# Kernel tuning notes

Hardware: AMD Instinct MI355X
Metric: run time of the kernel (lower is better)

Reference implementation:

```python
import jax, jax.numpy as jnp
import numpy as np

N_NODES = 100000
N_EDGES = 1600000
FEAT, HID, OUT = 256, 128, 64
N_BATCH = 10000
EPS = 1e-5


def gcn_conv(x, src, dst, W, b, n):
    # PyG GCNConv: linear -> add self loops -> sym-normalized scatter-add -> bias
    h = x @ W  # [N, C]
    loop = jnp.arange(n, dtype=src.dtype)
    s = jnp.concatenate([src, loop])
    d = jnp.concatenate([dst, loop])
    deg = jax.ops.segment_sum(jnp.ones_like(d, dtype=h.dtype), d, num_segments=n)
    dinv = jnp.where(deg > 0, jax.lax.rsqrt(deg), 0.0)
    norm = dinv[s] * dinv[d]                    # [E+N]
    msg = h[s] * norm[:, None]                  # gather + scale
    out = jax.ops.segment_sum(msg, d, num_segments=n)  # scatter-add
    return out + b


def batch_norm(x, gamma, beta):
    # training-mode BatchNorm1d: batch statistics, biased variance
    mu = jnp.mean(x, axis=0)
    var = jnp.var(x, axis=0)
    return (x - mu) * jax.lax.rsqrt(var + EPS) * gamma + beta


def setup_inputs() -> dict:
    key = jax.random.key(0)
    ks = jax.random.split(key, 8)
    features = jax.random.normal(ks[0], (N_NODES, FEAT), dtype=jnp.float32)
    edge_index = jax.random.randint(ks[1], (2, N_EDGES), 0, N_NODES, dtype=jnp.int64 if jax.config.jax_enable_x64 else jnp.int32)
    batch_nodes = jax.random.randint(ks[2], (N_BATCH,), 0, N_NODES, dtype=jnp.int32)
    W1 = jax.random.normal(ks[3], (FEAT, HID), dtype=jnp.float32) * (1.0 / np.sqrt(FEAT))
    b1 = jnp.zeros((HID,), jnp.float32)
    gamma1 = jnp.ones((HID,), jnp.float32)
    beta1 = jnp.zeros((HID,), jnp.float32)
    W2 = jax.random.normal(ks[4], (HID, OUT), dtype=jnp.float32) * (1.0 / np.sqrt(HID))
    b2 = jnp.zeros((OUT,), jnp.float32)
    gamma2 = jnp.ones((OUT,), jnp.float32)
    beta2 = jnp.zeros((OUT,), jnp.float32)
    return {"features": features, "edge_index": edge_index, "batch_nodes": batch_nodes,
            "W1": W1, "b1": b1, "gamma1": gamma1, "beta1": beta1,
            "W2": W2, "b2": b2, "gamma2": gamma2, "beta2": beta2}


def reference(features, edge_index, batch_nodes, W1, b1, gamma1, beta1, W2, b2, gamma2, beta2):
    src, dst = edge_index[0], edge_index[1]
    n = features.shape[0]
    x = gcn_conv(features, src, dst, W1, b1, n)
    x = jax.nn.relu(batch_norm(x, gamma1, beta1))
    # dropout treated as identity (deterministic reference)
    x = gcn_conv(x, src, dst, W2, b2, n)
    x = jax.nn.relu(batch_norm(x, gamma2, beta2))
    return jax.nn.log_softmax(x[batch_nodes], axis=1)
```

## Files before the change

### kernel.cpp

```cpp
#include <hip/hip_runtime.h>
#include <stdint.h>

typedef unsigned short bf16_t;

constexpr int kNN   = 100000;
constexpr int kNE   = 1600000;
constexpr int kFEAT = 256;
constexpr int kHID  = 128;
constexpr int kOUT  = 64;
constexpr int kNB   = 10000;
constexpr float kEPS = 1e-5f;

constexpr int kEPB  = 4096;
constexpr int kNBLK = (kNE + kEPB - 1) / kEPB;
constexpr int kNBUK = (kNN + 511) / 512;

typedef __attribute__((ext_vector_type(8))) short short8v;
typedef __attribute__((ext_vector_type(4))) float f32x4;

__device__ __forceinline__ float bf2f(bf16_t u) {
    union { uint32_t i; float f; } v; v.i = ((uint32_t)u) << 16; return v.f;
}
__device__ __forceinline__ bf16_t f2bf(float f) {
    uint32_t u = __float_as_uint(f);
    uint32_t r = (u + 0x7FFFu + ((u >> 16) & 1u)) >> 16;
    return (bf16_t)r;
}
__device__ __forceinline__ float lo16(uint32_t u) {
    union { uint32_t i; float f; } v; v.i = u << 16; return v.f;
}
__device__ __forceinline__ float hi16(uint32_t u) {
    union { uint32_t i; float f; } v; v.i = u & 0xFFFF0000u; return v.f;
}

__global__ void k_probe(const uint32_t* __restrict__ feat, const uint32_t* __restrict__ ei,
                        int* __restrict__ flags) {
    if (blockIdx.x == 0 && threadIdx.x == 0) {
        int good = 0;
        for (int j = 0; j < 256; j++) {
            uint32_t u = feat[j];
            uint32_t e = (u >> 7) & 0xFFu;
            if (e >= 100u && e <= 132u) good++;
        }
        flags[0] = (good > 128) ? 1 : 0;
        int zeros = 0;
        for (int j = 0; j < 128; j++) {
            if (ei[2 * j + 1] == 0u) zeros++;
        }
        flags[1] = (zeros > 64) ? 1 : 0;
    }
}


__global__ void k_hist1(const int* __restrict__ ei, const int* __restrict__ flags,
                        unsigned int* __restrict__ counts) {
    __shared__ unsigned int lh[kNBUK];
    int t = threadIdx.x;
    for (int i = t; i < kNBUK; i += 256) lh[i] = 0u;
    __syncthreads();
    int i64 = flags[1];
    int base = blockIdx.x * kEPB;
    for (int k = 0; k < 16; k++) {
        int e = base + k * 256 + t;
        if (e < kNE) {
            int d = i64 ? ei[2 * (kNE + e)] : ei[kNE + e];
            atomicAdd(&lh[d >> 9], 1u);
        }
    }
    __syncthreads();
    for (int i = t; i < kNBUK; i += 256) counts[(size_t)i * kNBLK + blockIdx.x] = lh[i];
}

__global__ void k_scanA(const unsigned int* __restrict__ counts, unsigned int* __restrict__ base,
                        float* __restrict__ stats) {
    __shared__ unsigned int ss[256];
    int t = threadIdx.x;
    for (int i = t; i < 384; i += 256) stats[i] = 0.f;
    unsigned int tot = 0u;
    if (t < kNBUK) {
        const unsigned int* row = counts + (size_t)t * kNBLK;
        for (int j = 0; j < kNBLK; j++) tot += row[j];
    }
    ss[t] = tot;
    __syncthreads();
    for (int o = 1; o < 256; o <<= 1) {
        unsigned int x = (t >= o) ? ss[t - o] : 0u;
        __syncthreads();
        ss[t] += x;
        __syncthreads();
    }
    if (t < kNBUK) base[t] = ss[t] - tot;
    if (t == 0) base[kNBUK] = ss[255];
}

__global__ void k_scanB(const unsigned int* __restrict__ counts, const unsigned int* __restrict__ base,
                        unsigned int* __restrict__ off) {
    __shared__ unsigned int ss[64];
    int b = blockIdx.x, t = threadIdx.x;
    unsigned int run = base[b];
    for (int c0 = 0; c0 < kNBLK; c0 += 64) {
        int idx = c0 + t;
        unsigned int v = (idx < kNBLK) ? counts[(size_t)b * kNBLK + idx] : 0u;
        ss[t] = v;
        __syncthreads();
        for (int o = 1; o < 64; o <<= 1) {
            unsigned int x = (t >= o) ? ss[t - o] : 0u;
            __syncthreads();
            ss[t] += x;
            __syncthreads();
        }
        if (idx < kNBLK) off[(size_t)b * kNBLK + idx] = run + ss[t] - v;
        unsigned int ctot = ss[63];
        __syncthreads();
        run += ctot;
    }
}

__global__ void k_scatter1(const int* __restrict__ ei, const int* __restrict__ flags,
                           const unsigned int* __restrict__ off, unsigned int* __restrict__ pairs) {
    __shared__ unsigned int lcur[kNBUK];
    int t = threadIdx.x;
    for (int i = t; i < kNBUK; i += 256) lcur[i] = off[(size_t)i * kNBLK + blockIdx.x];
    __syncthreads();
    int i64 = flags[1];
    int base = blockIdx.x * kEPB;
    for (int k = 0; k < 16; k++) {
        int e = base + k * 256 + t;
        if (e < kNE) {
            int s, d;
            if (i64) { s = ei[2 * e]; d = ei[2 * (kNE + e)]; }
            else     { s = ei[e];     d = ei[kNE + e]; }
            unsigned int p = atomicAdd(&lcur[d >> 9], 1u);
            pairs[p] = (unsigned int)s | ((unsigned int)(d & 511) << 17);
        }
    }
}

__global__ void __launch_bounds__(1024) k_scatter2(const unsigned int* __restrict__ pairs,
                        const unsigned int* __restrict__ base, unsigned int* __restrict__ deg,
                        float* __restrict__ dinv, unsigned int* __restrict__ cursor,
                        int* __restrict__ sorted) {
    __shared__ unsigned int hist[512], sc[512], lcur[512];
    int b = blockIdx.x, t = threadIdx.x;
    unsigned int gb = base[b];
    int cnt = (int)(base[b + 1] - gb);
    if (t < 512) hist[t] = 0u;
    __syncthreads();
    for (int i = t; i < cnt; i += 1024) atomicAdd(&hist[pairs[gb + i] >> 17], 1u);
    __syncthreads();
    if (t < 512) sc[t] = hist[t];
    __syncthreads();
    for (int o = 1; o < 512; o <<= 1) {
        unsigned int x = 0u;
        if (t < 512 && t >= o) x = sc[t - o];
        __syncthreads();
        if (t < 512) sc[t] += x;
        __syncthreads();
    }
    if (t < 512) {
        lcur[t] = gb + sc[t] - hist[t];
        int node = b * 512 + t;
        if (node < kNN) {
            unsigned int dg = hist[t] + 1u;
            deg[node] = dg;
            dinv[node] = rsqrtf((float)dg);
            cursor[node] = gb + sc[t];
        }
    }
    __syncthreads();
    for (int i = t; i < cnt; i += 1024) {
        unsigned int pk = pairs[gb + i];
        unsigned int slot = atomicAdd(&lcur[pk >> 17], 1u);
        sorted[slot] = (int)(pk & 0x1FFFFu);
    }
}


__global__ void k_prepw1(const void* __restrict__ W, const int* __restrict__ flags,
                         bf16_t* __restrict__ Wz) {
    int idx = blockIdx.x * 256 + threadIdx.x;
    if (idx >= 8 * 8 * 64) return;
    int l = idx & 63;
    int j = (idx >> 6) & 7;
    int t = idx >> 9;
    int col = j * 16 + (l & 15);
    int kb = t * 32 + (l >> 4) * 8;
    bf16_t o[8];
    if (flags[0]) {
        const bf16_t* Wb = (const bf16_t*)W;
        #pragma unroll
        for (int i = 0; i < 8; i++) o[i] = Wb[(size_t)(kb + i) * kHID + col];
    } else {
        const float* Wf = (const float*)W;
        #pragma unroll
        for (int i = 0; i < 8; i++) o[i] = f2bf(Wf[(size_t)(kb + i) * kHID + col]);
    }
    uint4 w;
    w.x = (uint32_t)o[0] | ((uint32_t)o[1] << 16);
    w.y = (uint32_t)o[2] | ((uint32_t)o[3] << 16);
    w.z = (uint32_t)o[4] | ((uint32_t)o[5] << 16);
    w.w = (uint32_t)o[6] | ((uint32_t)o[7] << 16);
    *(uint4*)(Wz + (size_t)idx * 8) = w;
}

__global__ void k_prepw2(const void* __restrict__ W, const int* __restrict__ flags,
                         bf16_t* __restrict__ Wz) {
    int idx = blockIdx.x * 256 + threadIdx.x;
    if (idx >= 4 * 4 * 64) return;
    int l = idx & 63;
    int j = (idx >> 6) & 3;
    int t = idx >> 8;
    int col = j * 16 + (l & 15);
    int kb = t * 32 + (l >> 4) * 8;
    bf16_t o[8];
    if (flags[0]) {
        const bf16_t* Wb = (const bf16_t*)W;
        #pragma unroll
        for (int i = 0; i < 8; i++) o[i] = Wb[(size_t)(kb + i) * kOUT + col];
    } else {
        const float* Wf = (const float*)W;
        #pragma unroll
        for (int i = 0; i < 8; i++) o[i] = f2bf(Wf[(size_t)(kb + i) * kOUT + col]);
    }
    uint4 w;
    w.x = (uint32_t)o[0] | ((uint32_t)o[1] << 16);
    w.y = (uint32_t)o[2] | ((uint32_t)o[3] << 16);
    w.z = (uint32_t)o[4] | ((uint32_t)o[5] << 16);
    w.w = (uint32_t)o[6] | ((uint32_t)o[7] << 16);
    *(uint4*)(Wz + (size_t)idx * 8) = w;
}

__global__ void k_gemm1(const void* __restrict__ A, const bf16_t* __restrict__ Wz,
                        const float* __restrict__ dinv, bf16_t* __restrict__ H,
                        const int* __restrict__ flags) {
    int isbf = flags[0];
    int wv = threadIdx.x >> 6;
    int l  = threadIdx.x & 63;
    int kgrp = l >> 4;
    int rbase = blockIdx.x * 128 + wv * 32;
    int arow0 = rbase + (l & 15);
    int arow1 = arow0 + 16;
    const bf16_t* Ab = (const bf16_t*)A;
    const float*  Af = (const float*)A;
    const short8v* Wv = (const short8v*)Wz;

    f32x4 acc[2][8];
    #pragma unroll
    for (int m = 0; m < 2; m++)
        #pragma unroll
        for (int j = 0; j < 8; j++)
            acc[m][j] = (f32x4){0.f, 0.f, 0.f, 0.f};

    #pragma unroll
    for (int t = 0; t < 8; t++) {
        int kbase = t * 32 + kgrp * 8;
        short8v a0, a1;
        #pragma unroll
        for (int i = 0; i < 8; i++) { a0[i] = 0; a1[i] = 0; }
        if (arow0 < kNN) {
            if (isbf) {
                a0 = *(const short8v*)(Ab + (size_t)arow0 * kFEAT + kbase);
            } else {
                const float* p = Af + (size_t)arow0 * kFEAT + kbase;
                #pragma unroll
                for (int i = 0; i < 8; i++) a0[i] = (short)f2bf(p[i]);
            }
        }
        if (arow1 < kNN) {
            if (isbf) {
                a1 = *(const short8v*)(Ab + (size_t)arow1 * kFEAT + kbase);
            } else {
                const float* p = Af + (size_t)arow1 * kFEAT + kbase;
                #pragma unroll
                for (int i = 0; i < 8; i++) a1[i] = (short)f2bf(p[i]);
            }
        }
        #pragma unroll
        for (int j = 0; j < 8; j++) {
            short8v b = Wv[(t * 8 + j) * 64 + l];
            acc[0][j] = __builtin_amdgcn_mfma_f32_16x16x32_bf16(a0, b, acc[0][j], 0, 0, 0);
            acc[1][j] = __builtin_amdgcn_mfma_f32_16x16x32_bf16(a1, b, acc[1][j], 0, 0, 0);
        }
    }

    #pragma unroll
    for (int m = 0; m < 2; m++) {
        #pragma unroll
        for (int r = 0; r < 4; r++) {
            int orow = rbase + m * 16 + kgrp * 4 + r;
            if (orow < kNN) {
                float dn = dinv[orow];
                bf16_t* hp = H + (size_t)orow * kHID + (l & 15);
                #pragma unroll
                for (int j = 0; j < 8; j++) hp[j * 16] = f2bf(acc[m][j][r] * dn);
            }
        }
    }
}

__global__ void k_agg1(const bf16_t* __restrict__ H, const int* __restrict__ sorted,
                       const unsigned int* __restrict__ cursor, const unsigned int* __restrict__ deg,
                       const float* __restrict__ dinv, const void* __restrict__ bias,
                       const int* __restrict__ flags, float* __restrict__ Out) {
    int t = threadIdx.x;
    int local = t >> 6;
    int lane = t & 63;
    int c0 = lane * 2;
    int n = blockIdx.x * 4 + local;
    if (n >= kNN) return;
    const uint32_t* Hrow = (const uint32_t*)H;
    float dn = dinv[n];
    uint32_t hu = Hrow[(size_t)n * 64 + lane];
    float acc0 = lo16(hu), acc1 = hi16(hu);
    unsigned int e1 = cursor[n];
    unsigned int e = e1 - (deg[n] - 1u);
    int cnt = (int)(e1 - e);
    for (; cnt >= 4; cnt -= 4, e += 4) {
        int s0 = sorted[e], s1 = sorted[e + 1], s2 = sorted[e + 2], s3 = sorted[e + 3];
        uint32_t u0 = Hrow[(size_t)s0 * 64 + lane];
        uint32_t u1 = Hrow[(size_t)s1 * 64 + lane];
        uint32_t u2 = Hrow[(size_t)s2 * 64 + lane];
        uint32_t u3 = Hrow[(size_t)s3 * 64 + lane];
        acc0 += lo16(u0) + lo16(u1) + lo16(u2) + lo16(u3);
        acc1 += hi16(u0) + hi16(u1) + hi16(u2) + hi16(u3);
    }
    for (; cnt > 0; cnt--, e++) {
        uint32_t u = Hrow[(size_t)sorted[e] * 64 + lane];
        acc0 += lo16(u);
        acc1 += hi16(u);
    }
    float b0, b1v;
    if (flags[0]) { b0 = bf2f(((const bf16_t*)bias)[c0]); b1v = bf2f(((const bf16_t*)bias)[c0 + 1]); }
    else          { b0 = ((const float*)bias)[c0];        b1v = ((const float*)bias)[c0 + 1]; }
    float2 o; o.x = acc0 * dn + b0; o.y = acc1 * dn + b1v;
    *(float2*)(Out + (size_t)n * kHID + c0) = o;
}

__global__ void k_stat1(const float* __restrict__ A1, float* __restrict__ stats) {
    int c = threadIdx.x & 127;
    int r0 = threadIdx.x >> 7;
    int chunk = (kNN + gridDim.x - 1) / gridDim.x;
    int nbeg = blockIdx.x * chunk;
    int nend = nbeg + chunk; if (nend > kNN) nend = kNN;
    float s0 = 0.f, s1 = 0.f;
    for (int n = nbeg + r0; n < nend; n += 2) {
        float v = A1[(size_t)n * kHID + c];
        s0 += v; s1 += v * v;
    }
    atomicAdd(&stats[c], s0);
    atomicAdd(&stats[kHID + c], s1);
}

__global__ void k_bnrelu1(const float* __restrict__ A1, const float* __restrict__ stats,
                          const void* __restrict__ gamma, const void* __restrict__ beta,
                          const int* __restrict__ flags, bf16_t* __restrict__ X1) {
    size_t i = (size_t)blockIdx.x * 256 + threadIdx.x;
    if (i >= (size_t)kNN * kHID) return;
    int c = (int)(i & 127);
    float mu = stats[c] * (1.f / kNN);
    float var = stats[kHID + c] * (1.f / kNN) - mu * mu;
    float g, b;
    if (flags[0]) { g = bf2f(((const bf16_t*)gamma)[c]); b = bf2f(((const bf16_t*)beta)[c]); }
    else          { g = ((const float*)gamma)[c];        b = ((const float*)beta)[c]; }
    float v = (A1[i] - mu) * rsqrtf(var + kEPS) * g + b;
    X1[i] = f2bf(v > 0.f ? v : 0.f);
}

__global__ void k_gemm2(const bf16_t* __restrict__ A, const bf16_t* __restrict__ Wz,
                        const float* __restrict__ dinv, bf16_t* __restrict__ H) {
    int wv = threadIdx.x >> 6;
    int l  = threadIdx.x & 63;
    int kgrp = l >> 4;
    int rbase = blockIdx.x * 128 + wv * 32;
    int arow0 = rbase + (l & 15);
    int arow1 = arow0 + 16;
    const short8v* Wv = (const short8v*)Wz;

    f32x4 acc[2][4];
    #pragma unroll
    for (int m = 0; m < 2; m++)
        #pragma unroll
        for (int j = 0; j < 4; j++)
            acc[m][j] = (f32x4){0.f, 0.f, 0.f, 0.f};

    #pragma unroll
    for (int t = 0; t < 4; t++) {
        int kbase = t * 32 + kgrp * 8;
        short8v a0, a1;
        #pragma unroll
        for (int i = 0; i < 8; i++) { a0[i] = 0; a1[i] = 0; }
        if (arow0 < kNN) a0 = *(const short8v*)(A + (size_t)arow0 * kHID + kbase);
        if (arow1 < kNN) a1 = *(const short8v*)(A + (size_t)arow1 * kHID + kbase);
        #pragma unroll
        for (int j = 0; j < 4; j++) {
            short8v b = Wv[(t * 4 + j) * 64 + l];
            acc[0][j] = __builtin_amdgcn_mfma_f32_16x16x32_bf16(a0, b, acc[0][j], 0, 0, 0);
            acc[1][j] = __builtin_amdgcn_mfma_f32_16x16x32_bf16(a1, b, acc[1][j], 0, 0, 0);
        }
    }

    #pragma unroll
    for (int m = 0; m < 2; m++) {
        #pragma unroll
        for (int r = 0; r < 4; r++) {
            int orow = rbase + m * 16 + kgrp * 4 + r;
            if (orow < kNN) {
                float dn = dinv[orow];
                bf16_t* hp = H + (size_t)orow * kOUT + (l & 15);
                #pragma unroll
                for (int j = 0; j < 4; j++) hp[j * 16] = f2bf(acc[m][j][r] * dn);
            }
        }
    }
}

__global__ void k_agg2(const bf16_t* __restrict__ H, const int* __restrict__ sorted,
                       const unsigned int* __restrict__ cursor, const unsigned int* __restrict__ deg,
                       const float* __restrict__ dinv, const void* __restrict__ bias,
                       const int* __restrict__ flags, float* __restrict__ Out) {
    int t = threadIdx.x;
    int local = t >> 5;
    int lane = t & 31;
    int c0 = lane * 2;
    int n = blockIdx.x * 8 + local;
    if (n >= kNN) return;
    const uint32_t* Hrow = (const uint32_t*)H;
    float dn = dinv[n];
    uint32_t hu = Hrow[(size_t)n * 32 + lane];
    float acc0 = lo16(hu), acc1 = hi16(hu);
    unsigned int e1 = cursor[n];
    unsigned int e = e1 - (deg[n] - 1u);
    int cnt = (int)(e1 - e);
    for (; cnt >= 4; cnt -= 4, e += 4) {
        int s0 = sorted[e], s1 = sorted[e + 1], s2 = sorted[e + 2], s3 = sorted[e + 3];
        uint32_t u0 = Hrow[(size_t)s0 * 32 + lane];
        uint32_t u1 = Hrow[(size_t)s1 * 32 + lane];
        uint32_t u2 = Hrow[(size_t)s2 * 32 + lane];
        uint32_t u3 = Hrow[(size_t)s3 * 32 + lane];
        acc0 += lo16(u0) + lo16(u1) + lo16(u2) + lo16(u3);
        acc1 += hi16(u0) + hi16(u1) + hi16(u2) + hi16(u3);
    }
    for (; cnt > 0; cnt--, e++) {
        uint32_t u = Hrow[(size_t)sorted[e] * 32 + lane];
        acc0 += lo16(u);
        acc1 += hi16(u);
    }
    float b0, b1v;
    if (flags[0]) { b0 = bf2f(((const bf16_t*)bias)[c0]); b1v = bf2f(((const bf16_t*)bias)[c0 + 1]); }
    else          { b0 = ((const float*)bias)[c0];        b1v = ((const float*)bias)[c0 + 1]; }
    float2 o; o.x = acc0 * dn + b0; o.y = acc1 * dn + b1v;
    *(float2*)(Out + (size_t)n * kOUT + c0) = o;
}

__global__ void k_stat2(const float* __restrict__ A2, float* __restrict__ stats) {
    int c = threadIdx.x & 63;
    int r0 = threadIdx.x >> 6;
    int chunk = (kNN + gridDim.x - 1) / gridDim.x;
    int nbeg = blockIdx.x * chunk;
    int nend = nbeg + chunk; if (nend > kNN) nend = kNN;
    float s0 = 0.f, s1 = 0.f;
    for (int n = nbeg + r0; n < nend; n += 4) {
        float v = A2[(size_t)n * kOUT + c];
        s0 += v; s1 += v * v;
    }
    atomicAdd(&stats[256 + c], s0);
    atomicAdd(&stats[320 + c], s1);
}

__global__ void k_out(const float* __restrict__ A2, const float* __restrict__ stats,
                      const int* __restrict__ batch, const void* __restrict__ gamma,
                      const void* __restrict__ beta, const int* __restrict__ flags,
                      bf16_t* __restrict__ out) {
    int wid = threadIdx.x >> 6;
    int lane = threadIdx.x & 63;
    int i = blockIdx.x * 4 + wid;
    if (i >= kNB) return;
    int n = batch[i];
    int c = lane;
    float mu = stats[256 + c] * (1.f / kNN);
    float var = stats[320 + c] * (1.f / kNN) - mu * mu;
    float g, b;
    if (flags[0]) { g = bf2f(((const bf16_t*)gamma)[c]); b = bf2f(((const bf16_t*)beta)[c]); }
    else          { g = ((const float*)gamma)[c];        b = ((const float*)beta)[c]; }
    float v = (A2[(size_t)n * kOUT + c] - mu) * rsqrtf(var + kEPS) * g + b;
    v = v > 0.f ? v : 0.f;
    float m = v;
    for (int o = 32; o; o >>= 1) m = fmaxf(m, __shfl_xor(m, o));
    float ex = expf(v - m);
    float s = ex;
    for (int o = 32; o; o >>= 1) s += __shfl_xor(s, o);
    float r = v - m - logf(s);
    if (flags[0]) out[(size_t)i * kOUT + c] = f2bf(r);
    else ((float*)out)[(size_t)i * kOUT + c] = r;
}

static inline size_t align_up(size_t x, size_t a) { return (x + a - 1) & ~(a - 1); }

extern "C" void kernel_launch(void* const* d_in, const int* in_sizes, int n_in,
                              void* d_out, int out_size, void* d_ws, size_t ws_size,
                              hipStream_t stream) {
    (void)in_sizes; (void)n_in; (void)out_size; (void)ws_size;
    const void* feat = d_in[0];
    const int* ei    = (const int*)d_in[1];
    const int* batch = (const int*)d_in[2];
    const void* W1   = d_in[3];
    const void* b1   = d_in[4];
    const void* g1   = d_in[5];
    const void* be1  = d_in[6];
    const void* W2   = d_in[7];
    const void* b2   = d_in[8];
    const void* g2   = d_in[9];
    const void* be2  = d_in[10];

    char* ws = (char*)d_ws;
    size_t o = 0;
    int*          flags  = (int*)(ws + o);          o = align_up(o + 32, 256);
    unsigned int* deg    = (unsigned int*)(ws + o); o = align_up(o + (size_t)kNN * 4, 256);
    float*        dinv   = (float*)(ws + o);        o = align_up(o + (size_t)kNN * 4, 256);
    unsigned int* cursor = (unsigned int*)(ws + o); o = align_up(o + (size_t)kNN * 4, 256);
    float*        stats  = (float*)(ws + o);        o = align_up(o + 384 * 4, 256);
    int*          sorted = (int*)(ws + o);          o = align_up(o + (size_t)kNE * 4, 256);
    bf16_t*       h1     = (bf16_t*)(ws + o);       o = align_up(o + (size_t)kNN * kHID * 2, 256);
    float*        a1     = (float*)(ws + o);        o = align_up(o + (size_t)kNN * kHID * 4, 256);
    bf16_t*       wz1    = (bf16_t*)(ws + o);       o = align_up(o + (size_t)8 * 8 * 64 * 8 * 2, 256);
    bf16_t*       wz2    = (bf16_t*)(ws + o);       o = align_up(o + (size_t)4 * 4 * 64 * 8 * 2, 256);

    unsigned int* pairs  = (unsigned int*)h1;
    unsigned int* counts = (unsigned int*)a1;
    unsigned int* offm   = (unsigned int*)((char*)a1 + 512 * 1024);
    unsigned int* gbase  = (unsigned int*)((char*)a1 + 1024 * 1024);

    bf16_t*       x1 = h1;
    bf16_t*       h2 = (bf16_t*)a1;
    float*        a2 = (float*)((char*)a1 + 16u * 1024u * 1024u);

    bf16_t* outp = (bf16_t*)d_out;

    k_probe   <<<1, 64, 0, stream>>>((const uint32_t*)feat, (const uint32_t*)ei, flags);
    k_prepw1  <<<16, 256, 0, stream>>>(W1, flags, wz1);
    k_prepw2  <<<4, 256, 0, stream>>>(W2, flags, wz2);
    k_hist1   <<<kNBLK, 256, 0, stream>>>(ei, flags, counts);
    k_scanA   <<<1, 256, 0, stream>>>(counts, gbase, stats);
    k_scanB   <<<kNBUK, 64, 0, stream>>>(counts, gbase, offm);
    k_scatter1<<<kNBLK, 256, 0, stream>>>(ei, flags, offm, pairs);
    k_scatter2<<<kNBUK, 1024, 0, stream>>>(pairs, gbase, deg, dinv, cursor, sorted);

    k_gemm1  <<<(kNN + 127) / 128, 256, 0, stream>>>(feat, wz1, dinv, h1, flags);
    k_agg1   <<<(kNN + 3) / 4, 256, 0, stream>>>(h1, sorted, cursor, deg, dinv, b1, flags, a1);
    k_stat1  <<<256, 256, 0, stream>>>(a1, stats);
    k_bnrelu1<<<(kNN * kHID + 255) / 256, 256, 0, stream>>>(a1, stats, g1, be1, flags, x1);

    k_gemm2<<<(kNN + 127) / 128, 256, 0, stream>>>(x1, wz2, dinv, h2);
    k_agg2 <<<(kNN + 7) / 8, 256, 0, stream>>>(h2, sorted, cursor, deg, dinv, b2, flags, a2);
    k_stat2<<<256, 256, 0, stream>>>(a2, stats);

    k_out<<<(kNB + 3) / 4, 256, 0, stream>>>(a2, stats, batch, g2, be2, flags, outp);
}
```

Baseline: 533.6 us.

## Fuse BN stats into aggregation and BN+ReLU into second GEMM load

The aggregation kernels now accumulate per-channel sum and sum-of-squares in shared memory and flush them with atomics, which removes the separate stat passes. BatchNorm+ReLU for layer 1 is folded into the second GEMM's A-operand load through a precomputed scale/shift vector, which drops the bnrelu kernel and the bf16 intermediate. The gathers move to 16-byte loads per lane, with indices shared by shuffles within a 16- or 8-lane group, and the grid becomes grid-stride. The weight-prep kernels are merged and the probe is parallelised. The trade-offs are that the GEMM2 A read is now fp32 (twice the bytes), h2 uses a padded 256-element stride, and every node issues many shared-memory atomics.

```diff
diff --git a/kernel.cpp b/kernel.cpp
--- a/kernel.cpp
+++ b/kernel.cpp
@@ -33,20 +33,26 @@
     union { uint32_t i; float f; } v; v.i = u & 0xFFFF0000u; return v.f;
 }
 
+#define ACC8(u) do { \
+    acc[0] += lo16((u).x); acc[1] += hi16((u).x); \
+    acc[2] += lo16((u).y); acc[3] += hi16((u).y); \
+    acc[4] += lo16((u).z); acc[5] += hi16((u).z); \
+    acc[6] += lo16((u).w); acc[7] += hi16((u).w); } while (0)
+
 __global__ void k_probe(const uint32_t* __restrict__ feat, const uint32_t* __restrict__ ei,
                         int* __restrict__ flags) {
-    if (blockIdx.x == 0 && threadIdx.x == 0) {
-        int good = 0;
-        for (int j = 0; j < 256; j++) {
-            uint32_t u = feat[j];
-            uint32_t e = (u >> 7) & 0xFFu;
-            if (e >= 100u && e <= 132u) good++;
-        }
+    int l = threadIdx.x;
+    int good = 0;
+    for (int j = l; j < 256; j += 64) {
+        uint32_t e = (feat[j] >> 7) & 0xFFu;
+        if (e >= 100u && e <= 132u) good++;
+    }
+    for (int o = 32; o; o >>= 1) good += __shfl_xor(good, o);
+    int zeros = 0;
+    for (int j = l; j < 128; j += 64) zeros += (ei[2 * j + 1] == 0u) ? 1 : 0;
+    for (int o = 32; o; o >>= 1) zeros += __shfl_xor(zeros, o);
+    if (l == 0) {
         flags[0] = (good > 128) ? 1 : 0;
-        int zeros = 0;
-        for (int j = 0; j < 128; j++) {
-            if (ei[2 * j + 1] == 0u) zeros++;
-        }
         flags[1] = (zeros > 64) ? 1 : 0;
     }
 }
@@ -175,59 +181,54 @@
     }
 }
 
-
-__global__ void k_prepw1(const void* __restrict__ W, const int* __restrict__ flags,
-                         bf16_t* __restrict__ Wz) {
-    int idx = blockIdx.x * 256 + threadIdx.x;
-    if (idx >= 8 * 8 * 64) return;
-    int l = idx & 63;
-    int j = (idx >> 6) & 7;
-    int t = idx >> 9;
-    int col = j * 16 + (l & 15);
-    int kb = t * 32 + (l >> 4) * 8;
-    bf16_t o[8];
-    if (flags[0]) {
-        const bf16_t* Wb = (const bf16_t*)W;
-        #pragma unroll
-        for (int i = 0; i < 8; i++) o[i] = Wb[(size_t)(kb + i) * kHID + col];
-    } else {
-        const float* Wf = (const float*)W;
-        #pragma unroll
-        for (int i = 0; i < 8; i++) o[i] = f2bf(Wf[(size_t)(kb + i) * kHID + col]);
-    }
-    uint4 w;
-    w.x = (uint32_t)o[0] | ((uint32_t)o[1] << 16);
-    w.y = (uint32_t)o[2] | ((uint32_t)o[3] << 16);
-    w.z = (uint32_t)o[4] | ((uint32_t)o[5] << 16);
-    w.w = (uint32_t)o[6] | ((uint32_t)o[7] << 16);
-    *(uint4*)(Wz + (size_t)idx * 8) = w;
-}
-
-__global__ void k_prepw2(const void* __restrict__ W, const int* __restrict__ flags,
-                         bf16_t* __restrict__ Wz) {
-    int idx = blockIdx.x * 256 + threadIdx.x;
-    if (idx >= 4 * 4 * 64) return;
-    int l = idx & 63;
-    int j = (idx >> 6) & 3;
-    int t = idx >> 8;
-    int col = j * 16 + (l & 15);
-    int kb = t * 32 + (l >> 4) * 8;
-    bf16_t o[8];
-    if (flags[0]) {
-        const bf16_t* Wb = (const bf16_t*)W;
-        #pragma unroll
-        for (int i = 0; i < 8; i++) o[i] = Wb[(size_t)(kb + i) * kOUT + col];
-    } else {
-        const float* Wf = (const float*)W;
-        #pragma unroll
-        for (int i = 0; i < 8; i++) o[i] = f2bf(Wf[(size_t)(kb + i) * kOUT + col]);
-    }
-    uint4 w;
-    w.x = (uint32_t)o[0] | ((uint32_t)o[1] << 16);
-    w.y = (uint32_t)o[2] | ((uint32_t)o[3] << 16);
-    w.z = (uint32_t)o[4] | ((uint32_t)o[5] << 16);
-    w.w = (uint32_t)o[6] | ((uint32_t)o[7] << 16);
-    *(uint4*)(Wz + (size_t)idx * 8) = w;
+__global__ void k_prepw(const void* __restrict__ W1, const void* __restrict__ W2,
+                        const int* __restrict__ flags, bf16_t* __restrict__ Wz1,
+                        bf16_t* __restrict__ Wz2) {
+    int gid = blockIdx.x * 256 + threadIdx.x;
+    int isbf = flags[0];
+    if (gid < 4096) {
+        int idx = gid;
+        int l = idx & 63, j = (idx >> 6) & 7, t = idx >> 9;
+        int col = j * 16 + (l & 15);
+        int kb = t * 32 + (l >> 4) * 8;
+        bf16_t o[8];
+        if (isbf) {
+            const bf16_t* Wb = (const bf16_t*)W1;
+            #pragma unroll
+            for (int i = 0; i < 8; i++) o[i] = Wb[(size_t)(kb + i) * kHID + col];
+        } else {
+            const float* Wf = (const float*)W1;
+            #pragma unroll
+            for (int i = 0; i < 8; i++) o[i] = f2bf(Wf[(size_t)(kb + i) * kHID + col]);
+        }
+        uint4 w;
+        w.x = (uint32_t)o[0] | ((uint32_t)o[1] << 16);
+        w.y = (uint32_t)o[2] | ((uint32_t)o[3] << 16);
+        w.z = (uint32_t)o[4] | ((uint32_t)o[5] << 16);
+        w.w = (uint32_t)o[6] | ((uint32_t)o[7] << 16);
+        *(uint4*)(Wz1 + (size_t)idx * 8) = w;
+    } else if (gid < 4096 + 1024) {
+        int idx = gid - 4096;
+        int l = idx & 63, j = (idx >> 6) & 3, t = idx >> 8;
+        int col = j * 16 + (l & 15);
+        int kb = t * 32 + (l >> 4) * 8;
+        bf16_t o[8];
+        if (isbf) {
+            const bf16_t* Wb = (const bf16_t*)W2;
+            #pragma unroll
+            for (int i = 0; i < 8; i++) o[i] = Wb[(size_t)(kb + i) * kOUT + col];
+        } else {
+            const float* Wf = (const float*)W2;
+            #pragma unroll
+            for (int i = 0; i < 8; i++) o[i] = f2bf(Wf[(size_t)(kb + i) * kOUT + col]);
+        }
+        uint4 w;
+        w.x = (uint32_t)o[0] | ((uint32_t)o[1] << 16);
+        w.y = (uint32_t)o[2] | ((uint32_t)o[3] << 16);
+        w.z = (uint32_t)o[4] | ((uint32_t)o[5] << 16);
+        w.w = (uint32_t)o[6] | ((uint32_t)o[7] << 16);
+        *(uint4*)(Wz2 + (size_t)idx * 8) = w;
+    }
 }
 
 __global__ void k_gemm1(const void* __restrict__ A, const bf16_t* __restrict__ Wz,
@@ -301,73 +302,94 @@
 __global__ void k_agg1(const bf16_t* __restrict__ H, const int* __restrict__ sorted,
                        const unsigned int* __restrict__ cursor, const unsigned int* __restrict__ deg,
                        const float* __restrict__ dinv, const void* __restrict__ bias,
-                       const int* __restrict__ flags, float* __restrict__ Out) {
+                       const int* __restrict__ flags, float* __restrict__ Out,
+                       float* __restrict__ stats) {
+    __shared__ float ss[256];
     int t = threadIdx.x;
-    int local = t >> 6;
-    int lane = t & 63;
-    int c0 = lane * 2;
-    int n = blockIdx.x * 4 + local;
-    if (n >= kNN) return;
-    const uint32_t* Hrow = (const uint32_t*)H;
-    float dn = dinv[n];
-    uint32_t hu = Hrow[(size_t)n * 64 + lane];
-    float acc0 = lo16(hu), acc1 = hi16(hu);
-    unsigned int e1 = cursor[n];
-    unsigned int e = e1 - (deg[n] - 1u);
-    int cnt = (int)(e1 - e);
-    for (; cnt >= 4; cnt -= 4, e += 4) {
-        int s0 = sorted[e], s1 = sorted[e + 1], s2 = sorted[e + 2], s3 = sorted[e + 3];
-        uint32_t u0 = Hrow[(size_t)s0 * 64 + lane];
-        uint32_t u1 = Hrow[(size_t)s1 * 64 + lane];
-        uint32_t u2 = Hrow[(size_t)s2 * 64 + lane];
-        uint32_t u3 = Hrow[(size_t)s3 * 64 + lane];
-        acc0 += lo16(u0) + lo16(u1) + lo16(u2) + lo16(u3);
-        acc1 += hi16(u0) + hi16(u1) + hi16(u2) + hi16(u3);
-    }
-    for (; cnt > 0; cnt--, e++) {
-        uint32_t u = Hrow[(size_t)sorted[e] * 64 + lane];
-        acc0 += lo16(u);
-        acc1 += hi16(u);
-    }
-    float b0, b1v;
-    if (flags[0]) { b0 = bf2f(((const bf16_t*)bias)[c0]); b1v = bf2f(((const bf16_t*)bias)[c0 + 1]); }
-    else          { b0 = ((const float*)bias)[c0];        b1v = ((const float*)bias)[c0 + 1]; }
-    float2 o; o.x = acc0 * dn + b0; o.y = acc1 * dn + b1v;
-    *(float2*)(Out + (size_t)n * kHID + c0) = o;
-}
-
-__global__ void k_stat1(const float* __restrict__ A1, float* __restrict__ stats) {
-    int c = threadIdx.x & 127;
-    int r0 = threadIdx.x >> 7;
-    int chunk = (kNN + gridDim.x - 1) / gridDim.x;
-    int nbeg = blockIdx.x * chunk;
-    int nend = nbeg + chunk; if (nend > kNN) nend = kNN;
-    float s0 = 0.f, s1 = 0.f;
-    for (int n = nbeg + r0; n < nend; n += 2) {
-        float v = A1[(size_t)n * kHID + c];
-        s0 += v; s1 += v * v;
-    }
-    atomicAdd(&stats[c], s0);
-    atomicAdd(&stats[kHID + c], s1);
-}
-
-__global__ void k_bnrelu1(const float* __restrict__ A1, const float* __restrict__ stats,
-                          const void* __restrict__ gamma, const void* __restrict__ beta,
-                          const int* __restrict__ flags, bf16_t* __restrict__ X1) {
-    size_t i = (size_t)blockIdx.x * 256 + threadIdx.x;
-    if (i >= (size_t)kNN * kHID) return;
-    int c = (int)(i & 127);
+    ss[t] = 0.f;
+    __syncthreads();
+    int g16 = t & 15;
+    int grp = t >> 4;
+    int c0 = g16 * 8;
+    float bv[8];
+    if (flags[0]) {
+        const bf16_t* bb = (const bf16_t*)bias;
+        #pragma unroll
+        for (int j = 0; j < 8; j++) bv[j] = bf2f(bb[c0 + j]);
+    } else {
+        const float* bf = (const float*)bias;
+        #pragma unroll
+        for (int j = 0; j < 8; j++) bv[j] = bf[c0 + j];
+    }
+    for (int n0 = blockIdx.x * 16; n0 < kNN; n0 += gridDim.x * 16) {
+        int n = n0 + grp;
+        float acc[8];
+        uint4 hs = *(const uint4*)(H + (size_t)n * kHID + c0);
+        acc[0] = lo16(hs.x); acc[1] = hi16(hs.x);
+        acc[2] = lo16(hs.y); acc[3] = hi16(hs.y);
+        acc[4] = lo16(hs.z); acc[5] = hi16(hs.z);
+        acc[6] = lo16(hs.w); acc[7] = hi16(hs.w);
+        unsigned int e1 = cursor[n];
+        int cnt = (int)(deg[n] - 1u);
+        unsigned int e0 = e1 - (unsigned int)cnt;
+        for (int base = 0; base < cnt; base += 16) {
+            int idx = 0;
+            if (base + g16 < cnt) idx = sorted[e0 + base + g16];
+            int m = cnt - base; if (m > 16) m = 16;
+            int j = 0;
+            for (; j + 4 <= m; j += 4) {
+                int s0 = __shfl(idx, j, 16);
+                int s1 = __shfl(idx, j + 1, 16);
+                int s2 = __shfl(idx, j + 2, 16);
+                int s3 = __shfl(idx, j + 3, 16);
+                uint4 u0 = *(const uint4*)(H + (size_t)s0 * kHID + c0);
+                uint4 u1 = *(const uint4*)(H + (size_t)s1 * kHID + c0);
+                uint4 u2 = *(const uint4*)(H + (size_t)s2 * kHID + c0);
+                uint4 u3 = *(const uint4*)(H + (size_t)s3 * kHID + c0);
+                ACC8(u0); ACC8(u1); ACC8(u2); ACC8(u3);
+            }
+            for (; j < m; j++) {
+                int s = __shfl(idx, j, 16);
+                uint4 u = *(const uint4*)(H + (size_t)s * kHID + c0);
+                ACC8(u);
+            }
+        }
+        float dn = dinv[n];
+        float o[8];
+        #pragma unroll
+        for (int j = 0; j < 8; j++) o[j] = acc[j] * dn + bv[j];
+        float4 w0 = {o[0], o[1], o[2], o[3]};
+        float4 w1 = {o[4], o[5], o[6], o[7]};
+        *(float4*)(Out + (size_t)n * kHID + c0) = w0;
+        *(float4*)(Out + (size_t)n * kHID + c0 + 4) = w1;
+        #pragma unroll
+        for (int j = 0; j < 8; j++) {
+            atomicAdd(&ss[c0 + j], o[j]);
+            atomicAdd(&ss[128 + c0 + j], o[j] * o[j]);
+        }
+    }
+    __syncthreads();
+    atomicAdd(&stats[t], ss[t]);
+}
+
+__global__ void k_bnprep(const float* __restrict__ stats, const void* __restrict__ gamma,
+                         const void* __restrict__ beta, const int* __restrict__ flags,
+                         float* __restrict__ bnp) {
+    int c = threadIdx.x;
     float mu = stats[c] * (1.f / kNN);
-    float var = stats[kHID + c] * (1.f / kNN) - mu * mu;
+    float var = stats[128 + c] * (1.f / kNN) - mu * mu;
+    float rs = rsqrtf(var + kEPS);
     float g, b;
     if (flags[0]) { g = bf2f(((const bf16_t*)gamma)[c]); b = bf2f(((const bf16_t*)beta)[c]); }
     else          { g = ((const float*)gamma)[c];        b = ((const float*)beta)[c]; }
-    float v = (A1[i] - mu) * rsqrtf(var + kEPS) * g + b;
-    X1[i] = f2bf(v > 0.f ? v : 0.f);
-}
-
-__global__ void k_gemm2(const bf16_t* __restrict__ A, const bf16_t* __restrict__ Wz,
-                        const float* __restrict__ dinv, bf16_t* __restrict__ H) {
+    float sc = rs * g;
+    bnp[c] = sc;
+    bnp[128 + c] = b - mu * sc;
+}
+
+__global__ void k_gemm2(const float* A, const bf16_t* __restrict__ Wz,
+                        const float* __restrict__ dinv, const float* __restrict__ bnp,
+                        bf16_t* H ) {
     int wv = threadIdx.x >> 6;
     int l  = threadIdx.x & 63;
     int kgrp = l >> 4;
@@ -386,11 +408,39 @@
     #pragma unroll
     for (int t = 0; t < 4; t++) {
         int kbase = t * 32 + kgrp * 8;
+        float4 sa = *(const float4*)(bnp + kbase);
+        float4 sb = *(const float4*)(bnp + kbase + 4);
+        float4 ha = *(const float4*)(bnp + 128 + kbase);
+        float4 hb = *(const float4*)(bnp + 128 + kbase + 4);
         short8v a0, a1;
         #pragma unroll
         for (int i = 0; i < 8; i++) { a0[i] = 0; a1[i] = 0; }
-        if (arow0 < kNN) a0 = *(const short8v*)(A + (size_t)arow0 * kHID + kbase);
-        if (arow1 < kNN) a1 = *(const short8v*)(A + (size_t)arow1 * kHID + kbase);
+        if (arow0 < kNN) {
+            float4 f0 = *(const float4*)(A + (size_t)arow0 * kHID + kbase);
+            float4 f1 = *(const float4*)(A + (size_t)arow0 * kHID + kbase + 4);
+            float v;
+            v = f0.x * sa.x + ha.x; a0[0] = (short)f2bf(v > 0.f ? v : 0.f);
+            v = f0.y * sa.y + ha.y; a0[1] = (short)f2bf(v > 0.f ? v : 0.f);
+            v = f0.z * sa.z + ha.z; a0[2] = (short)f2bf(v > 0.f ? v : 0.f);
+            v = f0.w * sa.w + ha.w; a0[3] = (short)f2bf(v > 0.f ? v : 0.f);
+            v = f1.x * sb.x + hb.x; a0[4] = (short)f2bf(v > 0.f ? v : 0.f);
+            v = f1.y * sb.y + hb.y; a0[5] = (short)f2bf(v > 0.f ? v : 0.f);
+            v = f1.z * sb.z + hb.z; a0[6] = (short)f2bf(v > 0.f ? v : 0.f);
+            v = f1.w * sb.w + hb.w; a0[7] = (short)f2bf(v > 0.f ? v : 0.f);
+        }
+        if (arow1 < kNN) {
+            float4 f0 = *(const float4*)(A + (size_t)arow1 * kHID + kbase);
+            float4 f1 = *(const float4*)(A + (size_t)arow1 * kHID + kbase + 4);
+            float v;
+            v = f0.x * sa.x + ha.x; a1[0] = (short)f2bf(v > 0.f ? v : 0.f);
+            v = f0.y * sa.y + ha.y; a1[1] = (short)f2bf(v > 0.f ? v : 0.f);
+            v = f0.z * sa.z + ha.z; a1[2] = (short)f2bf(v > 0.f ? v : 0.f);
+            v = f0.w * sa.w + ha.w; a1[3] = (short)f2bf(v > 0.f ? v : 0.f);
+            v = f1.x * sb.x + hb.x; a1[4] = (short)f2bf(v > 0.f ? v : 0.f);
+            v = f1.y * sb.y + hb.y; a1[5] = (short)f2bf(v > 0.f ? v : 0.f);
+            v = f1.z * sb.z + hb.z; a1[6] = (short)f2bf(v > 0.f ? v : 0.f);
+            v = f1.w * sb.w + hb.w; a1[7] = (short)f2bf(v > 0.f ? v : 0.f);
+        }
         #pragma unroll
         for (int j = 0; j < 4; j++) {
             short8v b = Wv[(t * 4 + j) * 64 + l];
@@ -406,7 +456,7 @@
             int orow = rbase + m * 16 + kgrp * 4 + r;
             if (orow < kNN) {
                 float dn = dinv[orow];
-                bf16_t* hp = H + (size_t)orow * kOUT + (l & 15);
+                bf16_t* hp = H + (size_t)orow * 256 + (l & 15);
                 #pragma unroll
                 for (int j = 0; j < 4; j++) hp[j * 16] = f2bf(acc[m][j][r] * dn);
             }
@@ -417,54 +467,75 @@
 __global__ void k_agg2(const bf16_t* __restrict__ H, const int* __restrict__ sorted,
                        const unsigned int* __restrict__ cursor, const unsigned int* __restrict__ deg,
                        const float* __restrict__ dinv, const void* __restrict__ bias,
-                       const int* __restrict__ flags, float* __restrict__ Out) {
+                       const int* __restrict__ flags, float* __restrict__ Out,
+                       float* __restrict__ stats) {
+    __shared__ float ss[128];
     int t = threadIdx.x;
-    int local = t >> 5;
-    int lane = t & 31;
-    int c0 = lane * 2;
-    int n = blockIdx.x * 8 + local;
-    if (n >= kNN) return;
-    const uint32_t* Hrow = (const uint32_t*)H;
-    float dn = dinv[n];
-    uint32_t hu = Hrow[(size_t)n * 32 + lane];
-    float acc0 = lo16(hu), acc1 = hi16(hu);
-    unsigned int e1 = cursor[n];
-    unsigned int e = e1 - (deg[n] - 1u);
-    int cnt = (int)(e1 - e);
-    for (; cnt >= 4; cnt -= 4, e += 4) {
-        int s0 = sorted[e], s1 = sorted[e + 1], s2 = sorted[e + 2], s3 = sorted[e + 3];
-        uint32_t u0 = Hrow[(size_t)s0 * 32 + lane];
-        uint32_t u1 = Hrow[(size_t)s1 * 32 + lane];
-        uint32_t u2 = Hrow[(size_t)s2 * 32 + lane];
-        uint32_t u3 = Hrow[(size_t)s3 * 32 + lane];
-        acc0 += lo16(u0) + lo16(u1) + lo16(u2) + lo16(u3);
-        acc1 += hi16(u0) + hi16(u1) + hi16(u2) + hi16(u3);
-    }
-    for (; cnt > 0; cnt--, e++) {
-        uint32_t u = Hrow[(size_t)sorted[e] * 32 + lane];
-        acc0 += lo16(u);
-        acc1 += hi16(u);
-    }
-    float b0, b1v;
-    if (flags[0]) { b0 = bf2f(((const bf16_t*)bias)[c0]); b1v = bf2f(((const bf16_t*)bias)[c0 + 1]); }
-    else          { b0 = ((const float*)bias)[c0];        b1v = ((const float*)bias)[c0 + 1]; }
-    float2 o; o.x = acc0 * dn + b0; o.y = acc1 * dn + b1v;
-    *(float2*)(Out + (size_t)n * kOUT + c0) = o;
-}
-
-__global__ void k_stat2(const float* __restrict__ A2, float* __restrict__ stats) {
-    int c = threadIdx.x & 63;
-    int r0 = threadIdx.x >> 6;
-    int chunk = (kNN + gridDim.x - 1) / gridDim.x;
-    int nbeg = blockIdx.x * chunk;
-    int nend = nbeg + chunk; if (nend > kNN) nend = kNN;
-    float s0 = 0.f, s1 = 0.f;
-    for (int n = nbeg + r0; n < nend; n += 4) {
-        float v = A2[(size_t)n * kOUT + c];
-        s0 += v; s1 += v * v;
-    }
-    atomicAdd(&stats[256 + c], s0);
-    atomicAdd(&stats[320 + c], s1);
+    if (t < 128) ss[t] = 0.f;
+    __syncthreads();
+    int g8 = t & 7;
+    int grp = t >> 3;
+    int c0 = g8 * 8;
+    float bv[8];
+    if (flags[0]) {
+        const bf16_t* bb = (const bf16_t*)bias;
+        #pragma unroll
+        for (int j = 0; j < 8; j++) bv[j] = bf2f(bb[c0 + j]);
+    } else {
+        const float* bf = (const float*)bias;
+        #pragma unroll
+        for (int j = 0; j < 8; j++) bv[j] = bf[c0 + j];
+    }
+    for (int n0 = blockIdx.x * 32; n0 < kNN; n0 += gridDim.x * 32) {
+        int n = n0 + grp;
+        float acc[8];
+        uint4 hs = *(const uint4*)(H + (size_t)n * 256 + c0);
+        acc[0] = lo16(hs.x); acc[1] = hi16(hs.x);
+        acc[2] = lo16(hs.y); acc[3] = hi16(hs.y);
+        acc[4] = lo16(hs.z); acc[5] = hi16(hs.z);
+        acc[6] = lo16(hs.w); acc[7] = hi16(hs.w);
+        unsigned int e1 = cursor[n];
+        int cnt = (int)(deg[n] - 1u);
+        unsigned int e0 = e1 - (unsigned int)cnt;
+        for (int base = 0; base < cnt; base += 8) {
+            int idx = 0;
+            if (base + g8 < cnt) idx = sorted[e0 + base + g8];
+            int m = cnt - base; if (m > 8) m = 8;
+            int j = 0;
+            for (; j + 4 <= m; j += 4) {
+                int s0 = __shfl(idx, j, 8);
+                int s1 = __shfl(idx, j + 1, 8);
+                int s2 = __shfl(idx, j + 2, 8);
+                int s3 = __shfl(idx, j + 3, 8);
+                uint4 u0 = *(const uint4*)(H + (size_t)s0 * 256 + c0);
+                uint4 u1 = *(const uint4*)(H + (size_t)s1 * 256 + c0);
+                uint4 u2 = *(const uint4*)(H + (size_t)s2 * 256 + c0);
+                uint4 u3 = *(const uint4*)(H + (size_t)s3 * 256 + c0);
+                ACC8(u0); ACC8(u1); ACC8(u2); ACC8(u3);
+            }
+            for (; j < m; j++) {
+                int s = __shfl(idx, j, 8);
+                uint4 u = *(const uint4*)(H + (size_t)s * 256 + c0);
+                ACC8(u);
+            }
+        }
+        float dn = dinv[n];
+        float o[8];
+        #pragma unroll
+        for (int j = 0; j < 8; j++) o[j] = acc[j] * dn + bv[j];
+        float4 w0 = {o[0], o[1], o[2], o[3]};
+        float4 w1 = {o[4], o[5], o[6], o[7]};
+        *(float4*)(Out + (size_t)n * kOUT + c0) = w0;
+        *(float4*)(Out + (size_t)n * kOUT + c0 + 4) = w1;
+        #pragma unroll
+        for (int j = 0; j < 8; j++) {
+            atomicAdd(&ss[c0 + j], o[j]);
+            atomicAdd(&ss[64 + c0 + j], o[j] * o[j]);
+        }
+    }
+    __syncthreads();
+    if (t < 64)  atomicAdd(&stats[256 + t], ss[t]);
+    else if (t < 128) atomicAdd(&stats[320 + (t - 64)], ss[t]);
 }
 
 __global__ void k_out(const float* __restrict__ A2, const float* __restrict__ stats,
@@ -519,6 +590,7 @@
     float*        dinv   = (float*)(ws + o);        o = align_up(o + (size_t)kNN * 4, 256);
     unsigned int* cursor = (unsigned int*)(ws + o); o = align_up(o + (size_t)kNN * 4, 256);
     float*        stats  = (float*)(ws + o);        o = align_up(o + 384 * 4, 256);
+    float*        bnp    = (float*)(ws + o);        o = align_up(o + 256 * 4, 256);
     int*          sorted = (int*)(ws + o);          o = align_up(o + (size_t)kNE * 4, 256);
     bf16_t*       h1     = (bf16_t*)(ws + o);       o = align_up(o + (size_t)kNN * kHID * 2, 256);
     float*        a1     = (float*)(ws + o);        o = align_up(o + (size_t)kNN * kHID * 4, 256);
@@ -530,29 +602,25 @@
     unsigned int* offm   = (unsigned int*)((char*)a1 + 512 * 1024);
     unsigned int* gbase  = (unsigned int*)((char*)a1 + 1024 * 1024);
 
-    bf16_t*       x1 = h1;
     bf16_t*       h2 = (bf16_t*)a1;
-    float*        a2 = (float*)((char*)a1 + 16u * 1024u * 1024u);
+    float*        a2 = (float*)h1;
 
     bf16_t* outp = (bf16_t*)d_out;
 
     k_probe   <<<1, 64, 0, stream>>>((const uint32_t*)feat, (const uint32_t*)ei, flags);
-    k_prepw1  <<<16, 256, 0, stream>>>(W1, flags, wz1);
-    k_prepw2  <<<4, 256, 0, stream>>>(W2, flags, wz2);
+    k_prepw   <<<20, 256, 0, stream>>>(W1, W2, flags, wz1, wz2);
     k_hist1   <<<kNBLK, 256, 0, stream>>>(ei, flags, counts);
     k_scanA   <<<1, 256, 0, stream>>>(counts, gbase, stats);
     k_scanB   <<<kNBUK, 64, 0, stream>>>(counts, gbase, offm);
     k_scatter1<<<kNBLK, 256, 0, stream>>>(ei, flags, offm, pairs);
     k_scatter2<<<kNBUK, 1024, 0, stream>>>(pairs, gbase, deg, dinv, cursor, sorted);
 
-    k_gemm1  <<<(kNN + 127) / 128, 256, 0, stream>>>(feat, wz1, dinv, h1, flags);
-    k_agg1   <<<(kNN + 3) / 4, 256, 0, stream>>>(h1, sorted, cursor, deg, dinv, b1, flags, a1);
-    k_stat1  <<<256, 256, 0, stream>>>(a1, stats);
-    k_bnrelu1<<<(kNN * kHID + 255) / 256, 256, 0, stream>>>(a1, stats, g1, be1, flags, x1);
-
-    k_gemm2<<<(kNN + 127) / 128, 256, 0, stream>>>(x1, wz2, dinv, h2);
-    k_agg2 <<<(kNN + 7) / 8, 256, 0, stream>>>(h2, sorted, cursor, deg, dinv, b2, flags, a2);
-    k_stat2<<<256, 256, 0, stream>>>(a2, stats);
+    k_gemm1 <<<(kNN + 127) / 128, 256, 0, stream>>>(feat, wz1, dinv, h1, flags);
+    k_agg1  <<<2048, 256, 0, stream>>>(h1, sorted, cursor, deg, dinv, b1, flags, a1, stats);
+    k_bnprep<<<1, 128, 0, stream>>>(stats, g1, be1, flags, bnp);
+
+    k_gemm2<<<(kNN + 127) / 128, 256, 0, stream>>>(a1, wz2, dinv, bnp, h2);
+    k_agg2 <<<1024, 256, 0, stream>>>(h2, sorted, cursor, deg, dinv, b2, flags, a2, stats);
 
     k_out<<<(kNB + 3) / 4, 256, 0, stream>>>(a2, stats, batch, g2, be2, flags, outp);
 }
```

After: 537.1 us. No clear change (+0.7%).
